# Kernel tuning notes

Measured on AMD Instinct MI355X. Metric: run time of the kernel, lower is better.

The kernel has to match this reference:

```python
import jax, jax.numpy as jnp
import numpy as np

N = 100000      # nodes
E = 1600000     # edges per node-kind graph
H = 2           # attention heads
F_IN = 64
F_OUT = 64
N_USER = 90000
D2 = 64
NB_CLASSES = 2


def setup_inputs() -> dict:
    key = jax.random.key(0)
    ks = jax.random.split(key, 16)
    xav = lambda k, shape: jax.random.normal(k, shape, jnp.float32) * np.sqrt(2.0 / (shape[-2] + shape[-1]))
    inp = {
        "h": jax.random.normal(ks[0], (N, F_IN), jnp.float32),
        "src0": jax.random.randint(ks[1], (E,), 0, N, jnp.int32),
        "trg0": jax.random.randint(ks[2], (E,), 0, N, jnp.int32),
        "src1": jax.random.randint(ks[3], (E,), 0, N, jnp.int32),
        "trg1": jax.random.randint(ks[4], (E,), 0, N, jnp.int32),
        # SpGATLayer params per node kind
        "w0": xav(ks[5], (H, F_IN, F_OUT)),
        "asrc0": xav(ks[6], (H, F_OUT)),   # attn_src squeezed from (H, F_OUT, 1)
        "atrg0": xav(ks[7], (H, F_OUT)),
        "w1": xav(ks[8], (H, F_IN, F_OUT)),
        "asrc1": xav(ks[9], (H, F_OUT)),
        "atrg1": xav(ks[10], (H, F_OUT)),
        # AdditiveAttention params (nn.Linear weights: [out, in])
        "aa_w1": xav(ks[11], (D2, F_IN)),
        "aa_w2": xav(ks[12], (D2, F_OUT)),
        "aa_m": xav(ks[13], (1, D2)),
        # final fc: in = d1 * (nb_node_kinds + 1) = 64 * 3
        "fc_w": xav(ks[14], (NB_CLASSES, F_OUT * 3)),
        "fc_b": jnp.zeros((NB_CLASSES,), jnp.float32),
        "n_user": N_USER,
    }
    return inp


def sp_gat_layer(h, w, a_src, a_trg, src, trg, n):
    # h: [N, F_IN]; w: [H, F_IN, F_OUT]
    hp = jnp.einsum("nf,hfo->hno", h, w)                  # [H, N, F_OUT]
    attn_src = jnp.einsum("hno,ho->nh", hp, a_src)        # [N, H]
    attn_trg = jnp.einsum("hno,ho->nh", hp, a_trg)        # [N, H]
    e = jax.nn.leaky_relu(attn_src[src] + attn_trg[trg], 0.2)  # [E, H]
    e = e - jnp.max(e)                                    # global max, as in source
    exp_e = jnp.exp(e)
    denom = jax.ops.segment_sum(exp_e, trg, num_segments=n)[trg] + 1e-16
    attn = (exp_e / denom)[:, :, None]                    # [E, H, 1]
    hp_nhf = jnp.transpose(hp, (1, 0, 2))                 # [N, H, F_OUT]
    h_weighted = hp_nhf[src] * attn                       # [E, H, F_OUT]
    out = jax.ops.segment_sum(h_weighted, trg, num_segments=n)  # [N, H, F_OUT]
    return out


def reference(h, src0, trg0, src1, trg1, w0, asrc0, atrg0, w1, asrc1, atrg1,
              aa_w1, aa_w2, aa_m, fc_w, fc_b, n_user):
    n = h.shape[0]
    # one SpGAT layer per node kind, then mean over heads (final-layer branch)
    x0 = sp_gat_layer(h, w0, asrc0, atrg0, src0, trg0, n).mean(axis=1)  # [N, F_OUT]
    x1 = sp_gat_layer(h, w1, asrc1, atrg1, src1, trg1, n).mean(axis=1)
    type_aware = jnp.stack([x0[:n_user], x1[:n_user]], axis=1)          # [n_user, 2, F_OUT]
    # AdditiveAttention
    feat = h[:n_user]                                                   # [n_user, F_IN]
    q = jnp.tanh(feat @ aa_w1.T[:, None, :].squeeze(1)[None][0] if False else
                 jnp.tanh(0.0))  # placeholder removed below
    q = jnp.tanh(feat[:, None, :] @ aa_w1.T + type_aware @ aa_w2.T)     # [n_user, 2, D2]
    scores = (q @ aa_m.T).squeeze(-1)                                   # [n_user, 2]
    beta = jax.nn.softmax(scores, axis=-1)
    type_fusion = jnp.einsum("nk,nkd->nd", beta, type_aware)[:, None, :]  # [n_user, 1, F_OUT]
    cat = jnp.concatenate([type_aware, type_fusion], axis=1).reshape(n_user, -1)  # [n_user, 3*F_OUT]
    logits = cat @ fc_w.T + fc_b
    return jax.nn.log_softmax(logits, axis=-1)
```

## Files before the change

### kernel.cpp

```cpp
#include <hip/hip_runtime.h>
#include <hip/hip_bf16.h>
#include <math.h>

#define N_NODES 100000
#define N_EDGES 1600000
#define N_USER  90000
#define NBUCK   256
#define BSZ     352
#define TILE    2048
#define TBLK    782
#define ACCB    22500
#define HPB     1024

typedef __attribute__((ext_vector_type(8))) short  short8;
typedef __attribute__((ext_vector_type(4))) float  floatx4;
typedef unsigned int  uint;
typedef unsigned short ushort;

__device__ __forceinline__ ushort f2bf(float x) {
  uint u = __float_as_uint(x);
  u += 0x7fffu + ((u >> 16) & 1u);
  return (ushort)(u >> 16);
}
__device__ __forceinline__ float bf2f(ushort v) { return __uint_as_float(((uint)v) << 16); }

__device__ __forceinline__ void split8(const float v[8], short8& hi, short8& lo) {
  #pragma unroll
  for (int j = 0; j < 8; ++j) {
    ushort h = f2bf(v[j]);
    hi[j] = (short)h;
    lo[j] = (short)f2bf(v[j] - bf2f(h));
  }
}
__device__ __forceinline__ void load_split8(const float* p, short8& hi, short8& lo) {
  const float4* q = (const float4*)p;
  float4 a = q[0], b = q[1];
  float v[8] = {a.x, a.y, a.z, a.w, b.x, b.y, b.z, b.w};
  split8(v, hi, lo);
}
__device__ __forceinline__ float fast_tanh(float x) {
  float t = __expf(2.f * x);
  return 1.f - 2.f / (t + 1.f);
}

__global__ __launch_bounds__(256) void stage1(
    const float* __restrict__ h,
    const float* __restrict__ wA,  const float* __restrict__ wB,
    const float* __restrict__ asA, const float* __restrict__ asB,
    const float* __restrict__ atA, const float* __restrict__ atB,
    uint* __restrict__ hpiA, uint* __restrict__ hpiB,
    float* __restrict__ attnsA, float* __restrict__ attnsB,
    float* __restrict__ attntA, float* __restrict__ attntB,
    const int* __restrict__ trgA, const int* __restrict__ trgB,
    int* __restrict__ bhist,
    int hpTot, int hpBase, int bhBase)
{
  __shared__ float part[4][16][4];
  __shared__ int hh[NBUCK];
  const int tid = threadIdx.x;

  if (blockIdx.x >= hpTot) {
    const int b2 = blockIdx.x - hpTot;
    const int layer = (b2 >= bhBase) ? 1 : 0;
    const int bid = b2 - layer * bhBase;
    const int* trg = layer ? trgB : trgA;
    int* bh = bhist + layer * NBUCK;
    hh[tid] = 0;
    __syncthreads();
    const int b0 = bid * TILE;
    #pragma unroll
    for (int j = 0; j < 8; ++j) {
      int e = b0 + j * 256 + tid;
      if (e < N_EDGES) {
        int t = trg[e];
        if (t < N_USER) atomicAdd(&hh[t / BSZ], 1);
      }
    }
    __syncthreads();
    if (hh[tid]) atomicAdd(&bh[tid], hh[tid]);
    return;
  }

  const int layer = (blockIdx.x >= hpBase) ? 1 : 0;
  const int bid = blockIdx.x - layer * hpBase;
  const float* w     = layer ? wB : wA;
  const float* a_src = layer ? asB : asA;
  const float* a_trg = layer ? atB : atA;
  uint*  hpi      = layer ? hpiB : hpiA;
  float* attn_src = layer ? attnsB : attnsA;
  float* attn_trg = layer ? attntB : attntA;

  const int lane = tid & 63, wv = tid >> 6;
  const int quad = lane >> 4, l15 = lane & 15;
  const int o = wv * 16 + l15;
  const float vas0 = a_src[o], vas1 = a_src[64 + o];
  const float vat0 = a_trg[o], vat1 = a_trg[64 + o];
  short8 b0h[2], b0l[2], b1h[2], b1l[2];
  #pragma unroll
  for (int ks = 0; ks < 2; ++ks) {
    float v0[8], v1[8];
    #pragma unroll
    for (int j = 0; j < 8; ++j) {
      int k = quad * 8 + j + ks * 32;
      v0[j] = w[k * 64 + o];
      v1[j] = w[4096 + k * 64 + o];
    }
    split8(v0, b0h[ks], b0l[ks]);
    split8(v1, b1h[ks], b1l[ks]);
  }
  for (int t = bid; t < N_NODES / 16; t += hpBase) {
    int m0 = t * 16, arow = m0 + l15;
    short8 ah[2], al[2];
    #pragma unroll
    for (int ks = 0; ks < 2; ++ks)
      load_split8(h + arow * 64 + quad * 8 + ks * 32, ah[ks], al[ks]);
    floatx4 c0 = {0.f, 0.f, 0.f, 0.f}, c1 = {0.f, 0.f, 0.f, 0.f};
    #pragma unroll
    for (int ks = 0; ks < 2; ++ks) {
      c0 = __builtin_amdgcn_mfma_f32_16x16x32_bf16(ah[ks], b0h[ks], c0, 0, 0, 0);
      c0 = __builtin_amdgcn_mfma_f32_16x16x32_bf16(ah[ks], b0l[ks], c0, 0, 0, 0);
      c0 = __builtin_amdgcn_mfma_f32_16x16x32_bf16(al[ks], b0h[ks], c0, 0, 0, 0);
      c1 = __builtin_amdgcn_mfma_f32_16x16x32_bf16(ah[ks], b1h[ks], c1, 0, 0, 0);
      c1 = __builtin_amdgcn_mfma_f32_16x16x32_bf16(ah[ks], b1l[ks], c1, 0, 0, 0);
      c1 = __builtin_amdgcn_mfma_f32_16x16x32_bf16(al[ks], b1h[ks], c1, 0, 0, 0);
    }
    #pragma unroll
    for (int r = 0; r < 4; ++r) {
      int n = m0 + quad * 4 + r;
      hpi[n * 64 + o] = (uint)f2bf(c0[r]) | ((uint)f2bf(c1[r]) << 16);
    }
    #pragma unroll
    for (int r = 0; r < 4; ++r) {
      float pas0 = c0[r] * vas0, pas1 = c1[r] * vas1;
      float pat0 = c0[r] * vat0, pat1 = c1[r] * vat1;
      #pragma unroll
      for (int m = 1; m < 16; m <<= 1) {
        pas0 += __shfl_xor(pas0, m, 64); pas1 += __shfl_xor(pas1, m, 64);
        pat0 += __shfl_xor(pat0, m, 64); pat1 += __shfl_xor(pat1, m, 64);
      }
      if (l15 == 0) {
        part[wv][quad * 4 + r][0] = pas0; part[wv][quad * 4 + r][1] = pas1;
        part[wv][quad * 4 + r][2] = pat0; part[wv][quad * 4 + r][3] = pat1;
      }
    }
    __syncthreads();
    if (tid < 64) {
      int row = tid & 15, which = tid >> 4;
      float v = part[0][row][which] + part[1][row][which]
              + part[2][row][which] + part[3][row][which];
      int n = m0 + row;
      if (which == 0)      attn_src[n * 2]     = v;
      else if (which == 1) attn_src[n * 2 + 1] = v;
      else if (which == 2) attn_trg[n * 2]     = v;
      else                 attn_trg[n * 2 + 1] = v;
    }
    __syncthreads();
  }
}

__global__ __launch_bounds__(256) void scanb2(const int* __restrict__ bhist,
                                              int* __restrict__ bstart, int* __restrict__ bcur)
{
  const int layer = blockIdx.x;
  const int* bh = bhist + layer * NBUCK;
  int* bs = bstart + layer * (NBUCK + 1);
  int* bc = bcur + layer * NBUCK * 16;
  __shared__ int s[256];
  int v = bh[threadIdx.x];
  s[threadIdx.x] = v;
  __syncthreads();
  for (int d = 1; d < 256; d <<= 1) {
    int t = (threadIdx.x >= d) ? s[threadIdx.x - d] : 0;
    __syncthreads();
    s[threadIdx.x] += t;
    __syncthreads();
  }
  int excl = s[threadIdx.x] - v;
  bs[threadIdx.x] = excl;
  bc[threadIdx.x * 16] = excl;
  if (threadIdx.x == 255) bs[256] = s[255];
}

__global__ __launch_bounds__(1024) void bucket2(
    const int* __restrict__ srcA, const int* __restrict__ srcB,
    const int* __restrict__ trgA, const int* __restrict__ trgB,
    int* __restrict__ bcur, uint* __restrict__ pairbufA, uint* __restrict__ pairbufB, int base)
{
  const int layer = (blockIdx.x >= base) ? 1 : 0;
  const int bid = blockIdx.x - layer * base;
  const int* src = layer ? srcB : srcA;
  const int* trg = layer ? trgB : trgA;
  int* bc = bcur + layer * NBUCK * 16;
  uint* pairbuf = layer ? pairbufB : pairbufA;

  __shared__ uint2 plds[TILE];
  __shared__ int bcnt[NBUCK], bscan[NBUCK], gbase[NBUCK];
  const int tid = threadIdx.x;
  const int b0 = bid * TILE;
  if (tid < NBUCK) bcnt[tid] = 0;
  __syncthreads();
  int myb[2], myr[2];
  uint myp[2];
  #pragma unroll
  for (int j = 0; j < 2; ++j) {
    int e = b0 + j * 1024 + tid;
    myb[j] = -1;
    if (e < N_EDGES) {
      int t = trg[e];
      if (t < N_USER) {
        int b = t / BSZ;
        int tl = t - b * BSZ;
        myb[j] = b;
        myr[j] = atomicAdd(&bcnt[b], 1);
        myp[j] = (uint)src[e] | ((uint)tl << 17);
      }
    }
  }
  __syncthreads();
  if (tid < NBUCK) {
    gbase[tid] = atomicAdd(&bc[tid * 16], bcnt[tid]);
    bscan[tid] = bcnt[tid];
  }
  __syncthreads();
  for (int d = 1; d < 256; d <<= 1) {
    int v = (tid >= d && tid < NBUCK) ? bscan[tid - d] : 0;
    __syncthreads();
    if (tid < NBUCK) bscan[tid] += v;
    __syncthreads();
  }
  #pragma unroll
  for (int j = 0; j < 2; ++j)
    if (myb[j] >= 0) plds[bscan[myb[j]] - bcnt[myb[j]] + myr[j]] = make_uint2(myp[j], (uint)myb[j]);
  __syncthreads();
  int total = bscan[NBUCK - 1];
  for (int i = tid; i < total; i += 1024) {
    uint2 pr = plds[i];
    int b = (int)pr.y;
    int idx = gbase[b] + (i - (bscan[b] - bcnt[b]));
    if (idx >= 0 && idx < N_EDGES) pairbuf[idx] = pr.x;
  }
}

__global__ __launch_bounds__(1024) void fine2(
    const uint* __restrict__ pairbufA, const uint* __restrict__ pairbufB,
    const int* __restrict__ bstart,
    int* __restrict__ offsA, int* __restrict__ offsB,
    int* __restrict__ csrA,  int* __restrict__ csrB,
    const float* __restrict__ attnsA, const float* __restrict__ attnsB,
    const float* __restrict__ attntA, const float* __restrict__ attntB,
    float2* __restrict__ wgtA, float2* __restrict__ wgtB, int base)
{
  const int layer = (blockIdx.x >= base) ? 1 : 0;
  const int b = blockIdx.x - layer * base;
  const uint* pairbuf = layer ? pairbufB : pairbufA;
  const int* bs = bstart + layer * (NBUCK + 1);
  int* offs = layer ? offsB : offsA;
  int* csr_src = layer ? csrB : csrA;
  const float* attn_src = layer ? attnsB : attnsA;
  const float* attn_trg = layer ? attntB : attntA;
  float2* wgt = layer ? wgtB : wgtA;

  __shared__ int cnt[BSZ + 1];
  __shared__ int cur[BSZ];
  __shared__ float lat[BSZ][2];
  const int tid = threadIdx.x;
  const int t0 = b * BSZ;
  const int nt = min(BSZ, N_USER - t0);
  const int pbeg = bs[b], pend = bs[b + 1];
  const float2* as2 = (const float2*)attn_src;
  const float2* at2 = (const float2*)attn_trg;
  for (int j = tid; j <= BSZ; j += 1024) cnt[j] = 0;
  for (int j = tid; j < BSZ; j += 1024) {
    float2 v = at2[min(t0 + j, N_USER - 1)];
    lat[j][0] = v.x; lat[j][1] = v.y;
  }
  __syncthreads();
  for (int i = pbeg + tid; i < pend; i += 1024) {
    int tl = min((int)(pairbuf[i] >> 17), BSZ - 1);
    atomicAdd(&cnt[tl], 1);
  }
  __syncthreads();
  if (tid == 0) {
    int run = 0;
    for (int j = 0; j < nt; ++j) { int c = cnt[j]; cnt[j] = run; run += c; }
    cnt[nt] = run;
  }
  __syncthreads();
  for (int j = tid; j < nt; j += 1024) {
    offs[t0 + j] = pbeg + cnt[j];
    cur[j] = cnt[j];
  }
  if (tid == 0 && t0 + nt == N_USER) offs[N_USER] = pbeg + cnt[nt];
  __syncthreads();
  for (int i = pbeg + tid; i < pend; i += 1024) {
    uint v = pairbuf[i];
    int s = min((int)(v & 0x1FFFFu), N_NODES - 1);
    int tl = min((int)(v >> 17), BSZ - 1);
    float2 as = as2[s];
    float e0 = as.x + lat[tl][0]; e0 = (e0 > 0.f) ? e0 : 0.2f * e0;
    float e1 = as.y + lat[tl][1]; e1 = (e1 > 0.f) ? e1 : 0.2f * e1;
    int p = pbeg + atomicAdd(&cur[tl], 1);
    p = min(max(p, 0), N_EDGES - 1);
    csr_src[p] = s;
    wgt[p] = make_float2(__expf(e0), __expf(e1));
  }
}

__global__ __launch_bounds__(256) void accum2(
    const int* __restrict__ offsA, const int* __restrict__ offsB,
    const int* __restrict__ csrA,  const int* __restrict__ csrB,
    const float2* __restrict__ wgtA, const float2* __restrict__ wgtB,
    const uint* __restrict__ hpiA, const uint* __restrict__ hpiB,
    float* __restrict__ xA, float* __restrict__ xB, int base, int swz)
{
  int layer, bid;
  if (swz) {
    const int xcd = blockIdx.x & 7, idx = blockIdx.x >> 3;
    layer = xcd >> 2;
    bid = idx * 4 + (xcd & 3);
  } else {
    layer = (blockIdx.x >= base) ? 1 : 0;
    bid = blockIdx.x - layer * base;
  }
  const int* offs = layer ? offsB : offsA;
  const int* csr_src = layer ? csrB : csrA;
  const float2* wgt = layer ? wgtB : wgtA;
  const uint* hpi = layer ? hpiB : hpiA;
  float* x = layer ? xB : xA;

  const int lane = threadIdx.x & 63, wv = threadIdx.x >> 6;
  int n = bid * 4 + wv;
  if (n >= N_USER) return;
  int beg = max(0, offs[n]);
  int end = min(offs[n + 1], N_EDGES);
  beg = __builtin_amdgcn_readfirstlane(beg);
  end = __builtin_amdgcn_readfirstlane(end);
  int deg = end - beg;
  float acc0 = 0.f, acc1 = 0.f, den0 = 0.f, den1 = 0.f;
  for (int base2 = 0; base2 < deg; base2 += 64) {
    int rem = min(64, deg - base2);
    int sv = csr_src[beg + base2 + min(lane, rem - 1)];
    sv = min(max(sv, 0), N_NODES - 1);
    int nfull = rem & ~7;
    for (int j = 0; j < nfull; j += 8) {
      int ss[8]; uint pv[8]; float2 W[8];
      #pragma unroll
      for (int u = 0; u < 8; ++u) ss[u] = __builtin_amdgcn_readlane(sv, j + u);
      #pragma unroll
      for (int u = 0; u < 8; ++u) pv[u] = (hpi + (size_t)ss[u] * 64)[lane];
      #pragma unroll
      for (int u = 0; u < 8; ++u) W[u] = wgt[beg + base2 + j + u];
      #pragma unroll
      for (int u = 0; u < 8; ++u) {
        den0 += W[u].x; den1 += W[u].y;
        acc0 += W[u].x * bf2f((ushort)(pv[u] & 0xffffu));
        acc1 += W[u].y * bf2f((ushort)(pv[u] >> 16));
      }
    }
    if (nfull < rem) {
      int j = nfull;
      int ss[8]; uint pv[8]; float2 W[8];
      #pragma unroll
      for (int u = 0; u < 8; ++u) ss[u] = __builtin_amdgcn_readlane(sv, min(j + u, rem - 1));
      #pragma unroll
      for (int u = 0; u < 8; ++u) pv[u] = (hpi + (size_t)ss[u] * 64)[lane];
      #pragma unroll
      for (int u = 0; u < 8; ++u)
        W[u] = (j + u < rem) ? wgt[beg + base2 + j + u] : make_float2(0.f, 0.f);
      #pragma unroll
      for (int u = 0; u < 8; ++u) {
        den0 += W[u].x; den1 += W[u].y;
        acc0 += W[u].x * bf2f((ushort)(pv[u] & 0xffffu));
        acc1 += W[u].y * bf2f((ushort)(pv[u] >> 16));
      }
    }
  }
  x[n * 64 + lane] = 0.5f * (acc0 / (den0 + 1e-16f) + acc1 / (den1 + 1e-16f));
}

__global__ __launch_bounds__(256) void final_mfma(
    const float* __restrict__ h, const float* __restrict__ x0, const float* __restrict__ x1,
    const float* __restrict__ aa_w1, const float* __restrict__ aa_w2, const float* __restrict__ aa_m,
    const float* __restrict__ fc_w, const float* __restrict__ fc_b, float* __restrict__ out)
{
  __shared__ float aam_s[64], fcw_s[384], fcb_s[2];
  __shared__ float scw0[2][4][16], scw1[2][4][16];
  const int tid = threadIdx.x;
  if (tid < 64)  aam_s[tid] = aa_m[tid];
  for (int i = tid; i < 384; i += 256) fcw_s[i] = fc_w[i];
  if (tid < 2)   fcb_s[tid] = fc_b[tid];
  const int lane = tid & 63, wv = tid >> 6, quad = lane >> 4, l15 = lane & 15;
  const int d = wv * 16 + l15;
  short8 b1h[2], b1l[2], b2h[2], b2l[2];
  #pragma unroll
  for (int ks = 0; ks < 2; ++ks) {
    load_split8(aa_w1 + d * 64 + quad * 8 + ks * 32, b1h[ks], b1l[ks]);
    load_split8(aa_w2 + d * 64 + quad * 8 + ks * 32, b2h[ks], b2l[ks]);
  }
  __syncthreads();
  int pp = 0;
  for (int t = blockIdx.x; t < N_USER / 16; t += gridDim.x) {
    int m0 = t * 16, arow = m0 + l15;
    const int erow = m0 + wv * 4 + quad;
    float4 ev0 = *(const float4*)(x0 + erow * 64 + l15 * 4);
    float4 ev1 = *(const float4*)(x1 + erow * 64 + l15 * 4);
    short8 ahh[2], ahl[2], a0h[2], a0l[2], a1h[2], a1l[2];
    #pragma unroll
    for (int ks = 0; ks < 2; ++ks) {
      load_split8(h  + arow * 64 + quad * 8 + ks * 32, ahh[ks], ahl[ks]);
      load_split8(x0 + arow * 64 + quad * 8 + ks * 32, a0h[ks], a0l[ks]);
      load_split8(x1 + arow * 64 + quad * 8 + ks * 32, a1h[ks], a1l[ks]);
    }
    floatx4 t1a = {0.f,0.f,0.f,0.f}, t20a = {0.f,0.f,0.f,0.f}, t21a = {0.f,0.f,0.f,0.f};
    #pragma unroll
    for (int ks = 0; ks < 2; ++ks) {
      t1a  = __builtin_amdgcn_mfma_f32_16x16x32_bf16(ahh[ks], b1h[ks], t1a, 0, 0, 0);
      t1a  = __builtin_amdgcn_mfma_f32_16x16x32_bf16(ahh[ks], b1l[ks], t1a, 0, 0, 0);
      t1a  = __builtin_amdgcn_mfma_f32_16x16x32_bf16(ahl[ks], b1h[ks], t1a, 0, 0, 0);
      t20a = __builtin_amdgcn_mfma_f32_16x16x32_bf16(a0h[ks], b2h[ks], t20a, 0, 0, 0);
      t20a = __builtin_amdgcn_mfma_f32_16x16x32_bf16(a0h[ks], b2l[ks], t20a, 0, 0, 0);
      t20a = __builtin_amdgcn_mfma_f32_16x16x32_bf16(a0l[ks], b2h[ks], t20a, 0, 0, 0);
      t21a = __builtin_amdgcn_mfma_f32_16x16x32_bf16(a1h[ks], b2h[ks], t21a, 0, 0, 0);
      t21a = __builtin_amdgcn_mfma_f32_16x16x32_bf16(a1h[ks], b2l[ks], t21a, 0, 0, 0);
      t21a = __builtin_amdgcn_mfma_f32_16x16x32_bf16(a1l[ks], b2h[ks], t21a, 0, 0, 0);
    }
    float am = aam_s[d];
    #pragma unroll
    for (int r = 0; r < 4; ++r) {
      float q0 = fast_tanh(t1a[r] + t20a[r]);
      float q1 = fast_tanh(t1a[r] + t21a[r]);
      float p0 = q0 * am, p1 = q1 * am;
      #pragma unroll
      for (int m = 1; m < 16; m <<= 1) { p0 += __shfl_xor(p0, m, 64); p1 += __shfl_xor(p1, m, 64); }
      if (l15 == 0) { scw0[pp][wv][quad * 4 + r] = p0; scw1[pp][wv][quad * 4 + r] = p1; }
    }
    __syncthreads();
    {
      int row = wv * 4 + quad, n = m0 + row;
      float s0 = scw0[pp][0][row] + scw0[pp][1][row] + scw0[pp][2][row] + scw0[pp][3][row];
      float s1 = scw1[pp][0][row] + scw1[pp][1][row] + scw1[pp][2][row] + scw1[pp][3][row];
      float mx = fmaxf(s0, s1);
      float e0 = __expf(s0 - mx), e1 = __expf(s1 - mx);
      float inv = 1.f / (e0 + e1);
      float b0 = e0 * inv, b1 = e1 * inv;
      float a0[4] = {ev0.x, ev0.y, ev0.z, ev0.w};
      float a1[4] = {ev1.x, ev1.y, ev1.z, ev1.w};
      float pc0 = 0.f, pc1 = 0.f;
      #pragma unroll
      for (int c = 0; c < 4; ++c) {
        int o = l15 * 4 + c;
        float fv = b0 * a0[c] + b1 * a1[c];
        pc0 += fcw_s[o] * a0[c] + fcw_s[64 + o] * a1[c] + fcw_s[128 + o] * fv;
        pc1 += fcw_s[192 + o] * a0[c] + fcw_s[256 + o] * a1[c] + fcw_s[320 + o] * fv;
      }
      #pragma unroll
      for (int m = 1; m < 16; m <<= 1) { pc0 += __shfl_xor(pc0, m, 64); pc1 += __shfl_xor(pc1, m, 64); }
      if (l15 == 0) {
        float l0 = pc0 + fcb_s[0], l1 = pc1 + fcb_s[1];
        float lm = fmaxf(l0, l1);
        float lse = lm + logf(__expf(l0 - lm) + __expf(l1 - lm));
        out[n * 2] = l0 - lse;
        out[n * 2 + 1] = l1 - lse;
      }
    }
    pp ^= 1;
  }
}

extern "C" void kernel_launch(void* const* d_in, const int* in_sizes, int n_in,
                              void* d_out, int out_size, void* d_ws, size_t ws_size,
                              hipStream_t stream)
{
  const float* h     = (const float*)d_in[0];
  const int*   src0  = (const int*)d_in[1];
  const int*   trg0  = (const int*)d_in[2];
  const int*   src1  = (const int*)d_in[3];
  const int*   trg1  = (const int*)d_in[4];
  const float* w0    = (const float*)d_in[5];
  const float* asrc0 = (const float*)d_in[6];
  const float* atrg0 = (const float*)d_in[7];
  const float* w1    = (const float*)d_in[8];
  const float* asrc1 = (const float*)d_in[9];
  const float* atrg1 = (const float*)d_in[10];
  const float* aa_w1 = (const float*)d_in[11];
  const float* aa_w2 = (const float*)d_in[12];
  const float* aa_m  = (const float*)d_in[13];
  const float* fc_w  = (const float*)d_in[14];
  const float* fc_b  = (const float*)d_in[15];
  float* out = (float*)d_out;

  const int nl = (ws_size >= (size_t)162 * 1024 * 1024) ? 2 : 1;
  const size_t L = (size_t)(nl - 1);

  char* ws = (char*)d_ws;
  size_t off = 0;
  auto alloc = [&](size_t bytes) -> void* {
    void* p = ws + off;
    off = (off + bytes + 255) & ~(size_t)255;
    return p;
  };
  uint*   hpi      = (uint*)alloc((size_t)nl * N_NODES * 64 * 4);
  float*  attn_src = (float*)alloc((size_t)nl * N_NODES * 2 * 4);
  float*  attn_trg = (float*)alloc((size_t)nl * N_NODES * 2 * 4);
  float*  x0       = (float*)alloc((size_t)N_USER * 64 * 4);
  float*  x1       = (float*)alloc((size_t)N_USER * 64 * 4);
  int*    offs     = (int*)alloc((size_t)nl * (N_USER + 1) * 4);
  int*    csr      = (int*)alloc((size_t)nl * N_EDGES * 4);
  uint*   pairbuf  = (uint*)alloc((size_t)nl * N_EDGES * 4);
  float2* wgt      = (float2*)alloc((size_t)nl * N_EDGES * 8);
  int*    bhist    = (int*)alloc((size_t)2 * NBUCK * 4);
  int*    bstart   = (int*)alloc((size_t)2 * (NBUCK + 1) * 4);
  int*    bcur     = (int*)alloc((size_t)2 * NBUCK * 16 * 4);

  uint*   hpi1     = hpi + L * (size_t)N_NODES * 64;
  float*  attns1   = attn_src + L * (size_t)N_NODES * 2;
  float*  attnt1   = attn_trg + L * (size_t)N_NODES * 2;
  int*    offs1    = offs + L * (size_t)(N_USER + 1);
  int*    csr1     = csr + L * (size_t)N_EDGES;
  uint*   pairbuf1 = pairbuf + L * (size_t)N_EDGES;
  float2* wgt1     = wgt + L * (size_t)N_EDGES;

  if (nl == 2) {
    hipMemsetAsync(bhist, 0, (size_t)2 * NBUCK * 4, stream);
    hipLaunchKernelGGL(stage1, dim3(2 * HPB + 2 * TBLK), dim3(256), 0, stream,
                       h, w0, w1, asrc0, asrc1, atrg0, atrg1,
                       hpi, hpi1, attn_src, attns1, attn_trg, attnt1,
                       trg0, trg1, bhist, 2 * HPB, HPB, TBLK);
    hipLaunchKernelGGL(scanb2, dim3(2), dim3(256), 0, stream, bhist, bstart, bcur);
    hipLaunchKernelGGL(bucket2, dim3(2 * TBLK), dim3(1024), 0, stream,
                       src0, src1, trg0, trg1, bcur, pairbuf, pairbuf1, TBLK);
    hipLaunchKernelGGL(fine2, dim3(2 * NBUCK), dim3(1024), 0, stream,
                       pairbuf, pairbuf1, bstart, offs, offs1, csr, csr1,
                       attn_src, attns1, attn_trg, attnt1, wgt, wgt1, NBUCK);
    hipLaunchKernelGGL(accum2, dim3(2 * ACCB), dim3(256), 0, stream,
                       offs, offs1, csr, csr1, wgt, wgt1, hpi, hpi1, x0, x1, ACCB, 1);
  } else {
    for (int layer = 0; layer < 2; ++layer) {
      const float* w    = layer ? w1 : w0;
      const float* asrc = layer ? asrc1 : asrc0;
      const float* atrg = layer ? atrg1 : atrg0;
      const int*   src  = layer ? src1 : src0;
      const int*   trg  = layer ? trg1 : trg0;
      float*       x    = layer ? x1 : x0;
      hipMemsetAsync(bhist, 0, (size_t)NBUCK * 4, stream);
      hipLaunchKernelGGL(stage1, dim3(HPB + TBLK), dim3(256), 0, stream,
                         h, w, w, asrc, asrc, atrg, atrg,
                         hpi, hpi, attn_src, attn_src, attn_trg, attn_trg,
                         trg, trg, bhist, HPB, HPB, TBLK);
      hipLaunchKernelGGL(scanb2, dim3(1), dim3(256), 0, stream, bhist, bstart, bcur);
      hipLaunchKernelGGL(bucket2, dim3(TBLK), dim3(1024), 0, stream,
                         src, src, trg, trg, bcur, pairbuf, pairbuf, TBLK);
      hipLaunchKernelGGL(fine2, dim3(NBUCK), dim3(1024), 0, stream,
                         pairbuf, pairbuf, bstart, offs, offs, csr, csr,
                         attn_src, attn_src, attn_trg, attn_trg, wgt, wgt, NBUCK);
      hipLaunchKernelGGL(accum2, dim3(ACCB), dim3(256), 0, stream,
                         offs, offs, csr, csr, wgt, wgt, hpi, hpi, x, x, ACCB, 0);
    }
  }
  hipLaunchKernelGGL(final_mfma, dim3(1875), dim3(256), 0, stream,
                     h, x0, x1, aa_w1, aa_w2, aa_m, fc_w, fc_b, out);
}
```

Baseline: 422.8 us.

## Compute edge attention weights inside accumulation kernel instead of materializing them

Edge attention weights are no longer computed in the CSR-building kernel and stored to a per-edge float2 buffer. The accumulation kernel now gathers attn_src per edge with one lane per edge, applies leaky-relu and exp, reduces the denominator with a wave shuffle, and broadcasts the weights with readlane. This removes a 12.8 MB write and re-read of weights per layer and shrinks the workspace, which also lowers the threshold for the two-layer batched path. The cost is an extra random gather of attn_src plus the shuffle reduction inside the latency-bound accumulation loop.

```diff
diff --git a/kernel.cpp b/kernel.cpp
--- a/kernel.cpp
+++ b/kernel.cpp
@@ -245,10 +245,7 @@
     const uint* __restrict__ pairbufA, const uint* __restrict__ pairbufB,
     const int* __restrict__ bstart,
     int* __restrict__ offsA, int* __restrict__ offsB,
-    int* __restrict__ csrA,  int* __restrict__ csrB,
-    const float* __restrict__ attnsA, const float* __restrict__ attnsB,
-    const float* __restrict__ attntA, const float* __restrict__ attntB,
-    float2* __restrict__ wgtA, float2* __restrict__ wgtB, int base)
+    int* __restrict__ csrA,  int* __restrict__ csrB, int base)
 {
   const int layer = (blockIdx.x >= base) ? 1 : 0;
   const int b = blockIdx.x - layer * base;
@@ -256,24 +253,14 @@
   const int* bs = bstart + layer * (NBUCK + 1);
   int* offs = layer ? offsB : offsA;
   int* csr_src = layer ? csrB : csrA;
-  const float* attn_src = layer ? attnsB : attnsA;
-  const float* attn_trg = layer ? attntB : attntA;
-  float2* wgt = layer ? wgtB : wgtA;
 
   __shared__ int cnt[BSZ + 1];
   __shared__ int cur[BSZ];
-  __shared__ float lat[BSZ][2];
   const int tid = threadIdx.x;
   const int t0 = b * BSZ;
   const int nt = min(BSZ, N_USER - t0);
   const int pbeg = bs[b], pend = bs[b + 1];
-  const float2* as2 = (const float2*)attn_src;
-  const float2* at2 = (const float2*)attn_trg;
   for (int j = tid; j <= BSZ; j += 1024) cnt[j] = 0;
-  for (int j = tid; j < BSZ; j += 1024) {
-    float2 v = at2[min(t0 + j, N_USER - 1)];
-    lat[j][0] = v.x; lat[j][1] = v.y;
-  }
   __syncthreads();
   for (int i = pbeg + tid; i < pend; i += 1024) {
     int tl = min((int)(pairbuf[i] >> 17), BSZ - 1);
@@ -296,20 +283,17 @@
     uint v = pairbuf[i];
     int s = min((int)(v & 0x1FFFFu), N_NODES - 1);
     int tl = min((int)(v >> 17), BSZ - 1);
-    float2 as = as2[s];
-    float e0 = as.x + lat[tl][0]; e0 = (e0 > 0.f) ? e0 : 0.2f * e0;
-    float e1 = as.y + lat[tl][1]; e1 = (e1 > 0.f) ? e1 : 0.2f * e1;
     int p = pbeg + atomicAdd(&cur[tl], 1);
     p = min(max(p, 0), N_EDGES - 1);
     csr_src[p] = s;
-    wgt[p] = make_float2(__expf(e0), __expf(e1));
   }
 }
 
 __global__ __launch_bounds__(256) void accum2(
     const int* __restrict__ offsA, const int* __restrict__ offsB,
     const int* __restrict__ csrA,  const int* __restrict__ csrB,
-    const float2* __restrict__ wgtA, const float2* __restrict__ wgtB,
+    const float* __restrict__ attnsA, const float* __restrict__ attnsB,
+    const float* __restrict__ attntA, const float* __restrict__ attntB,
     const uint* __restrict__ hpiA, const uint* __restrict__ hpiB,
     float* __restrict__ xA, float* __restrict__ xB, int base, int swz)
 {
@@ -324,7 +308,8 @@
   }
   const int* offs = layer ? offsB : offsA;
   const int* csr_src = layer ? csrB : csrA;
-  const float2* wgt = layer ? wgtB : wgtA;
+  const float2* as2 = (const float2*)(layer ? attnsB : attnsA);
+  const float2* at2 = (const float2*)(layer ? attntB : attntA);
   const uint* hpi = layer ? hpiB : hpiA;
   float* x = layer ? xB : xA;
 
@@ -336,42 +321,39 @@
   beg = __builtin_amdgcn_readfirstlane(beg);
   end = __builtin_amdgcn_readfirstlane(end);
   int deg = end - beg;
+  const float2 at = at2[n];
   float acc0 = 0.f, acc1 = 0.f, den0 = 0.f, den1 = 0.f;
   for (int base2 = 0; base2 < deg; base2 += 64) {
     int rem = min(64, deg - base2);
     int sv = csr_src[beg + base2 + min(lane, rem - 1)];
     sv = min(max(sv, 0), N_NODES - 1);
-    int nfull = rem & ~7;
-    for (int j = 0; j < nfull; j += 8) {
-      int ss[8]; uint pv[8]; float2 W[8];
+    float2 as = as2[sv];
+    float e0 = as.x + at.x; e0 = (e0 > 0.f) ? e0 : 0.2f * e0;
+    float e1 = as.y + at.y; e1 = (e1 > 0.f) ? e1 : 0.2f * e1;
+    float wx = (lane < rem) ? __expf(e0) : 0.f;
+    float wy = (lane < rem) ? __expf(e1) : 0.f;
+    {
+      float dx = wx, dy = wy;
+      #pragma unroll
+      for (int m = 1; m < 64; m <<= 1) { dx += __shfl_xor(dx, m, 64); dy += __shfl_xor(dy, m, 64); }
+      den0 += dx; den1 += dy;
+    }
+    const int wxi = __float_as_int(wx), wyi = __float_as_int(wy);
+    for (int j = 0; j < rem; j += 8) {
+      int ss[8]; uint pv[8]; float Wx[8], Wy[8];
       #pragma unroll
       for (int u = 0; u < 8; ++u) ss[u] = __builtin_amdgcn_readlane(sv, j + u);
       #pragma unroll
       for (int u = 0; u < 8; ++u) pv[u] = (hpi + (size_t)ss[u] * 64)[lane];
       #pragma unroll
-      for (int u = 0; u < 8; ++u) W[u] = wgt[beg + base2 + j + u];
-      #pragma unroll
       for (int u = 0; u < 8; ++u) {
-        den0 += W[u].x; den1 += W[u].y;
-        acc0 += W[u].x * bf2f((ushort)(pv[u] & 0xffffu));
-        acc1 += W[u].y * bf2f((ushort)(pv[u] >> 16));
-      }
-    }
-    if (nfull < rem) {
-      int j = nfull;
-      int ss[8]; uint pv[8]; float2 W[8];
-      #pragma unroll
-      for (int u = 0; u < 8; ++u) ss[u] = __builtin_amdgcn_readlane(sv, min(j + u, rem - 1));
-      #pragma unroll
-      for (int u = 0; u < 8; ++u) pv[u] = (hpi + (size_t)ss[u] * 64)[lane];
-      #pragma unroll
-      for (int u = 0; u < 8; ++u)
-        W[u] = (j + u < rem) ? wgt[beg + base2 + j + u] : make_float2(0.f, 0.f);
+        Wx[u] = __int_as_float(__builtin_amdgcn_readlane(wxi, j + u));
+        Wy[u] = __int_as_float(__builtin_amdgcn_readlane(wyi, j + u));
+      }
       #pragma unroll
       for (int u = 0; u < 8; ++u) {
-        den0 += W[u].x; den1 += W[u].y;
-        acc0 += W[u].x * bf2f((ushort)(pv[u] & 0xffffu));
-        acc1 += W[u].y * bf2f((ushort)(pv[u] >> 16));
+        acc0 += Wx[u] * bf2f((ushort)(pv[u] & 0xffffu));
+        acc1 += Wy[u] * bf2f((ushort)(pv[u] >> 16));
       }
     }
   }
@@ -489,7 +471,7 @@
   const float* fc_b  = (const float*)d_in[15];
   float* out = (float*)d_out;
 
-  const int nl = (ws_size >= (size_t)162 * 1024 * 1024) ? 2 : 1;
+  const int nl = (ws_size >= (size_t)140 * 1024 * 1024) ? 2 : 1;
   const size_t L = (size_t)(nl - 1);
 
   char* ws = (char*)d_ws;
@@ -507,7 +489,6 @@
   int*    offs     = (int*)alloc((size_t)nl * (N_USER + 1) * 4);
   int*    csr      = (int*)alloc((size_t)nl * N_EDGES * 4);
   uint*   pairbuf  = (uint*)alloc((size_t)nl * N_EDGES * 4);
-  float2* wgt      = (float2*)alloc((size_t)nl * N_EDGES * 8);
   int*    bhist    = (int*)alloc((size_t)2 * NBUCK * 4);
   int*    bstart   = (int*)alloc((size_t)2 * (NBUCK + 1) * 4);
   int*    bcur     = (int*)alloc((size_t)2 * NBUCK * 16 * 4);
@@ -518,7 +499,6 @@
   int*    offs1    = offs + L * (size_t)(N_USER + 1);
   int*    csr1     = csr + L * (size_t)N_EDGES;
   uint*   pairbuf1 = pairbuf + L * (size_t)N_EDGES;
-  float2* wgt1     = wgt + L * (size_t)N_EDGES;
 
   if (nl == 2) {
     hipMemsetAsync(bhist, 0, (size_t)2 * NBUCK * 4, stream);
@@ -530,10 +510,10 @@
     hipLaunchKernelGGL(bucket2, dim3(2 * TBLK), dim3(1024), 0, stream,
                        src0, src1, trg0, trg1, bcur, pairbuf, pairbuf1, TBLK);
     hipLaunchKernelGGL(fine2, dim3(2 * NBUCK), dim3(1024), 0, stream,
-                       pairbuf, pairbuf1, bstart, offs, offs1, csr, csr1,
-                       attn_src, attns1, attn_trg, attnt1, wgt, wgt1, NBUCK);
+                       pairbuf, pairbuf1, bstart, offs, offs1, csr, csr1, NBUCK);
     hipLaunchKernelGGL(accum2, dim3(2 * ACCB), dim3(256), 0, stream,
-                       offs, offs1, csr, csr1, wgt, wgt1, hpi, hpi1, x0, x1, ACCB, 1);
+                       offs, offs1, csr, csr1, attn_src, attns1, attn_trg, attnt1,
+                       hpi, hpi1, x0, x1, ACCB, 1);
   } else {
     for (int layer = 0; layer < 2; ++layer) {
       const float* w    = layer ? w1 : w0;
@@ -551,10 +531,10 @@
       hipLaunchKernelGGL(bucket2, dim3(TBLK), dim3(1024), 0, stream,
                          src, src, trg, trg, bcur, pairbuf, pairbuf, TBLK);
       hipLaunchKernelGGL(fine2, dim3(NBUCK), dim3(1024), 0, stream,
-                         pairbuf, pairbuf, bstart, offs, offs, csr, csr,
-                         attn_src, attn_src, attn_trg, attn_trg, wgt, wgt, NBUCK);
+                         pairbuf, pairbuf, bstart, offs, offs, csr, csr, NBUCK);
       hipLaunchKernelGGL(accum2, dim3(ACCB), dim3(256), 0, stream,
-                         offs, offs, csr, csr, wgt, wgt, hpi, hpi, x, x, ACCB, 0);
+                         offs, offs, csr, csr, attn_src, attn_src, attn_trg, attn_trg,
+                         hpi, hpi, x, x, ACCB, 0);
     }
   }
   hipLaunchKernelGGL(final_mfma, dim3(1875), dim3(256), 0, stream,
```

Result: faster. 400.2 us, median of 2 (-5.3%).
